# Kernel optimization log

Hardware: AMD Instinct MI355X
Metric: run time of the kernel (lower is better)

Reference implementation:

```python
import jax, jax.numpy as jnp
import numpy as np

GRID_H, GRID_W = 14, 14  # grid_size from init_kwargs (crop_height, crop_width)


def _bilinear_crop(feature_map, boxes, bbox_idx, crop_h, crop_w):
    """crop_and_resize-style ROIAlign.

    feature_map: [N, C, H, W] float
    boxes:       [M, 4] (x1, y1, x2, y2) in feature-map pixel coords
    bbox_idx:    [M] int32 batch index per box
    returns:     [M, C, crop_h, crop_w]
    """
    N, C, H, W = feature_map.shape
    x1, y1, x2, y2 = boxes[:, 0], boxes[:, 1], boxes[:, 2], boxes[:, 3]

    # Sample points evenly spaced INCLUDING the box corners (tf.crop_and_resize grid).
    ti = jnp.arange(crop_h, dtype=boxes.dtype) / (crop_h - 1)  # [gh]
    tj = jnp.arange(crop_w, dtype=boxes.dtype) / (crop_w - 1)  # [gw]
    ys = y1[:, None] + (y2 - y1)[:, None] * ti  # [M, gh]
    xs = x1[:, None] + (x2 - x1)[:, None] * tj  # [M, gw]

    # Out-of-range samples get extrapolation value 0.
    my = (ys >= 0) & (ys <= H - 1)  # [M, gh]
    mx = (xs >= 0) & (xs <= W - 1)  # [M, gw]

    y0f = jnp.floor(ys)
    x0f = jnp.floor(xs)
    ly = ys - y0f  # [M, gh] lerp weights
    lx = xs - x0f  # [M, gw]

    y0 = jnp.clip(y0f, 0, H - 1).astype(jnp.int32)
    y1i = jnp.clip(y0f + 1, 0, H - 1).astype(jnp.int32)
    x0 = jnp.clip(x0f, 0, W - 1).astype(jnp.int32)
    x1i = jnp.clip(x0f + 1, 0, W - 1).astype(jnp.int32)

    b = bbox_idx[:, None, None]            # [M,1,1]
    Y0, Y1 = y0[:, :, None], y1i[:, :, None]   # [M,gh,1]
    X0, X1 = x0[:, None, :], x1i[:, None, :]   # [M,1,gw]

    # Advanced indexing with the channel slice in the middle -> result [M,gh,gw,C]
    g00 = feature_map[b, :, Y0, X0]
    g01 = feature_map[b, :, Y0, X1]
    g10 = feature_map[b, :, Y1, X0]
    g11 = feature_map[b, :, Y1, X1]

    wy = ly[:, :, None, None]  # [M,gh,1,1]
    wx = lx[:, None, :, None]  # [M,1,gw,1]
    out = (g00 * (1 - wy) * (1 - wx) + g01 * (1 - wy) * wx
           + g10 * wy * (1 - wx) + g11 * wy * wx)  # [M,gh,gw,C]

    mask = (my[:, :, None] & mx[:, None, :])[..., None]  # [M,gh,gw,1]
    out = jnp.where(mask, out, jnp.zeros((), out.dtype))
    return jnp.transpose(out, (0, 3, 1, 2))  # [M,C,gh,gw]


def setup_inputs() -> dict:
    key = jax.random.key(0)
    k1, k2, k3, k4, k5, k6, k7 = jax.random.split(key, 7)
    N, C, H, W = 4, 256, 200, 200
    img = 800  # original image height/width; stride = img / H = 4
    M = 2048

    feature_map = jax.random.normal(k1, (N, C, H, W), dtype=jnp.float32)

    n = jax.random.randint(k2, (M,), 0, N).astype(jnp.float32)
    score = jax.random.uniform(k3, (M,), dtype=jnp.float32)
    x1 = jax.random.uniform(k4, (M,), dtype=jnp.float32, maxval=img * 0.6)
    y1 = jax.random.uniform(k5, (M,), dtype=jnp.float32, maxval=img * 0.6)
    bw = jax.random.uniform(k6, (M,), dtype=jnp.float32, minval=16.0, maxval=img * 0.4)
    bh = jax.random.uniform(k7, (M,), dtype=jnp.float32, minval=16.0, maxval=img * 0.4)
    x2 = jnp.minimum(x1 + bw, img - 1.0)
    y2 = jnp.minimum(y1 + bh, img - 1.0)

    rois = jnp.stack([n, score, x1, y1, x2, y2], axis=1)  # [M, 6]
    return {"feature_map": feature_map, "rois": rois, "img_height": img}


def reference(feature_map, rois, img_height):
    H = feature_map.shape[2]
    stride = img_height / H
    bbox_idx = rois[:, 0].astype(jnp.int32)
    boxes = rois[:, 2:] / stride  # image coords -> feature-map coords
    return _bilinear_crop(feature_map, boxes, bbox_idx, GRID_H, GRID_W)
```

## Files before the change

kernel.cpp:

```cpp
#include <hip/hip_runtime.h>

#define GH 14
#define GW 14

__global__ __launch_bounds__(256) void nchw_to_nhwc_kernel(
    const float* __restrict__ src, float* __restrict__ dst, int C, int HW)
{
    __shared__ float tile[32][33];
    const int b  = blockIdx.z;
    const int p0 = blockIdx.x * 32;
    const int c0 = blockIdx.y * 32;
    const int tx = threadIdx.x;
    const int ty = threadIdx.y;
    const float* s = src + (size_t)b * C * HW;
    float*       d = dst + (size_t)b * C * HW;
    #pragma unroll
    for (int k = 0; k < 4; ++k)
        tile[ty + k * 8][tx] = s[(size_t)(c0 + ty + k * 8) * HW + p0 + tx];
    __syncthreads();
    #pragma unroll
    for (int k = 0; k < 4; ++k)
        d[(size_t)(p0 + ty + k * 8) * C + c0 + tx] = tile[tx][ty + k * 8];
}

__global__ __launch_bounds__(256) void roi_gather_nhwc_kernel(
    const float* __restrict__ fmapT,
    const float* __restrict__ rois,
    const int*   __restrict__ imgh,
    float*       __restrict__ out,
    int C, int H, int W)
{
    __shared__ float lds[64 * 197];
    const int tid  = threadIdx.x;
    const int lane = tid & 63;
    const int wv   = tid >> 6;
    const int m    = blockIdx.y;
    const int c0   = blockIdx.x * 64;

    const float stride = (float)imgh[0] / (float)H;
    const float* r = rois + (size_t)m * 6;
    const int   b   = (int)r[0];
    const float rx1 = r[2] / stride;
    const float ry1 = r[3] / stride;
    const float rx2 = r[4] / stride;
    const float ry2 = r[5] / stride;

    const float* __restrict__ base = fmapT + (size_t)b * H * W * C + c0 + lane;

    const float fH = (float)(H - 1), fW = (float)(W - 1);

    #pragma unroll 2
    for (int k = 0; k < 49; ++k) {
        const int s = wv * 49 + k;
        const int i = s / GW;
        const int j = s - i * GW;

        const float ys = ry1 + (ry2 - ry1) * ((float)i / (float)(GH - 1));
        const float xs = rx1 + (rx2 - rx1) * ((float)j / (float)(GW - 1));

        const bool my = (ys >= 0.0f) && (ys <= fH);
        const bool mx = (xs >= 0.0f) && (xs <= fW);

        const float y0f = floorf(ys);
        const float x0f = floorf(xs);
        const float ly  = ys - y0f;
        const float lx  = xs - x0f;

        const int y0  = (int)fminf(fmaxf(y0f,        0.0f), fH);
        const int y1i = (int)fminf(fmaxf(y0f + 1.0f, 0.0f), fH);
        const int x0  = (int)fminf(fmaxf(x0f,        0.0f), fW);
        const int x1i = (int)fminf(fmaxf(x0f + 1.0f, 0.0f), fW);

        const float msk = (my && mx) ? 1.0f : 0.0f;
        const float w00 = msk * (1.0f - ly) * (1.0f - lx);
        const float w01 = msk * (1.0f - ly) * lx;
        const float w10 = msk * ly * (1.0f - lx);
        const float w11 = msk * ly * lx;

        const int o00 = (y0  * W + x0 ) * C;
        const int o01 = (y0  * W + x1i) * C;
        const int o10 = (y1i * W + x0 ) * C;
        const int o11 = (y1i * W + x1i) * C;
        const float g00 = base[o00];
        const float g01 = base[o01];
        const float g10 = base[o10];
        const float g11 = base[o11];

        lds[lane * 197 + s] = g00 * w00 + g01 * w01 + g10 * w10 + g11 * w11;
    }
    __syncthreads();

    for (int k = tid; k < 64 * GH * GW; k += 256) {
        const int ch = k / (GH * GW);
        const int s  = k - ch * (GH * GW);
        out[((size_t)m * C + c0 + ch) * (GH * GW) + s] = lds[ch * 197 + s];
    }
}

#define CCHUNK 64
__global__ __launch_bounds__(256) void roi_align_fallback(
    const float* __restrict__ fmap, const float* __restrict__ rois,
    const int* __restrict__ imgh, float* __restrict__ out, int C, int H, int W)
{
    const int t = threadIdx.x;
    if (t >= GH * GW) return;
    const int m = blockIdx.y;
    const int c0 = blockIdx.x * CCHUNK;
    const int j = t % GW;
    const int i = t / GW;
    const float stride = (float)imgh[0] / (float)H;
    const float* r = rois + (size_t)m * 6;
    const int b = (int)r[0];
    const float x1 = r[2] / stride, y1 = r[3] / stride;
    const float x2 = r[4] / stride, y2 = r[5] / stride;
    const float ys = y1 + (y2 - y1) * ((float)i / (float)(GH - 1));
    const float xs = x1 + (x2 - x1) * ((float)j / (float)(GW - 1));
    const bool my = (ys >= 0.0f) && (ys <= (float)(H - 1));
    const bool mx = (xs >= 0.0f) && (xs <= (float)(W - 1));
    const float y0f = floorf(ys), x0f = floorf(xs);
    const float ly = ys - y0f, lx = xs - x0f;
    const int y0  = (int)fminf(fmaxf(y0f,        0.0f), (float)(H - 1));
    const int y1i = (int)fminf(fmaxf(y0f + 1.0f, 0.0f), (float)(H - 1));
    const int x0  = (int)fminf(fmaxf(x0f,        0.0f), (float)(W - 1));
    const int x1i = (int)fminf(fmaxf(x0f + 1.0f, 0.0f), (float)(W - 1));
    const float msk = (my && mx) ? 1.0f : 0.0f;
    const float w00 = msk * (1.0f - ly) * (1.0f - lx);
    const float w01 = msk * (1.0f - ly) * lx;
    const float w10 = msk * ly * (1.0f - lx);
    const float w11 = msk * ly * lx;
    const int o00 = y0 * W + x0, o01 = y0 * W + x1i;
    const int o10 = y1i * W + x0, o11 = y1i * W + x1i;
    const int HW = H * W;
    const float* __restrict__ p = fmap + ((size_t)b * C + c0) * (size_t)HW;
    float* __restrict__ o = out + ((size_t)m * C + c0) * (size_t)(GH * GW) + t;
    #pragma unroll 4
    for (int c = 0; c < CCHUNK; ++c) {
        const float g00 = p[o00], g01 = p[o01], g10 = p[o10], g11 = p[o11];
        *o = g00 * w00 + g01 * w01 + g10 * w10 + g11 * w11;
        p += HW; o += GH * GW;
    }
}

extern "C" void kernel_launch(void* const* d_in, const int* in_sizes, int n_in,
                              void* d_out, int out_size, void* d_ws, size_t ws_size,
                              hipStream_t stream) {
    const float* fmap = (const float*)d_in[0];
    const float* rois = (const float*)d_in[1];
    const int*   imgh = (const int*)d_in[2];
    float* out = (float*)d_out;

    const int C = 256, H = 200, W = 200, N = 4;
    const int M  = in_sizes[1] / 6;
    const int HW = H * W;

    const size_t need = (size_t)N * C * HW * sizeof(float);
    if (ws_size >= need) {
        float* fmapT = (float*)d_ws;
        dim3 tgrid(HW / 32, C / 32, N);
        nchw_to_nhwc_kernel<<<tgrid, dim3(32, 8), 0, stream>>>(fmap, fmapT, C, HW);
        dim3 ggrid(C / 64, M);
        roi_gather_nhwc_kernel<<<ggrid, 256, 0, stream>>>(fmapT, rois, imgh, out, C, H, W);
    } else {
        dim3 grid(C / CCHUNK, M);
        roi_align_fallback<<<grid, 256, 0, stream>>>(fmap, rois, imgh, out, C, H, W);
    }
}
```

Before: 737.9 us.

## Gather all channels per ROI with float4 loads and precomputed sample tables

The gather kernel now runs one block per ROI covering all 256 channels. Sample offsets and bilinear weights are computed once into LDS tables, and each lane loads float4 vectors of four channels. Results are staged in LDS in passes of 28 samples, then transposed to write float4 rows of the NCHW output. This cuts redundant coordinate math and issues wider gather loads, at the cost of fewer, larger blocks and extra barriers per pass.

```diff
diff --git a/kernel.cpp b/kernel.cpp
--- a/kernel.cpp
+++ b/kernel.cpp
@@ -2,6 +2,9 @@
 
 #define GH 14
 #define GW 14
+#define GSAMP (GH * GW)
+#define PASS_S 28
+#define STG_STRIDE 260
 
 __global__ __launch_bounds__(256) void nchw_to_nhwc_kernel(
     const float* __restrict__ src, float* __restrict__ dst, int C, int HW)
@@ -23,19 +26,21 @@
         d[(size_t)(p0 + ty + k * 8) * C + c0 + tx] = tile[tx][ty + k * 8];
 }
 
-__global__ __launch_bounds__(256) void roi_gather_nhwc_kernel(
+__global__ __launch_bounds__(256, 4) void roi_gather_nhwc_kernel(
     const float* __restrict__ fmapT,
     const float* __restrict__ rois,
     const int*   __restrict__ imgh,
     float*       __restrict__ out,
     int C, int H, int W)
 {
-    __shared__ float lds[64 * 197];
+    __shared__ int4   s_oq[GSAMP];
+    __shared__ float4 s_w[GSAMP];
+    __shared__ float  stage[PASS_S * STG_STRIDE];
+
     const int tid  = threadIdx.x;
     const int lane = tid & 63;
     const int wv   = tid >> 6;
-    const int m    = blockIdx.y;
-    const int c0   = blockIdx.x * 64;
+    const int m    = blockIdx.x;
 
     const float stride = (float)imgh[0] / (float)H;
     const float* r = rois + (size_t)m * 6;
@@ -45,55 +50,72 @@
     const float rx2 = r[4] / stride;
     const float ry2 = r[5] / stride;
 
-    const float* __restrict__ base = fmapT + (size_t)b * H * W * C + c0 + lane;
-
+    const int C4 = C >> 2;
     const float fH = (float)(H - 1), fW = (float)(W - 1);
 
-    #pragma unroll 2
-    for (int k = 0; k < 49; ++k) {
-        const int s = wv * 49 + k;
-        const int i = s / GW;
-        const int j = s - i * GW;
-
+    if (tid < GSAMP) {
+        const int i = tid / GW;
+        const int j = tid - i * GW;
         const float ys = ry1 + (ry2 - ry1) * ((float)i / (float)(GH - 1));
         const float xs = rx1 + (rx2 - rx1) * ((float)j / (float)(GW - 1));
-
         const bool my = (ys >= 0.0f) && (ys <= fH);
         const bool mx = (xs >= 0.0f) && (xs <= fW);
-
         const float y0f = floorf(ys);
         const float x0f = floorf(xs);
         const float ly  = ys - y0f;
         const float lx  = xs - x0f;
-
         const int y0  = (int)fminf(fmaxf(y0f,        0.0f), fH);
         const int y1i = (int)fminf(fmaxf(y0f + 1.0f, 0.0f), fH);
         const int x0  = (int)fminf(fmaxf(x0f,        0.0f), fW);
         const int x1i = (int)fminf(fmaxf(x0f + 1.0f, 0.0f), fW);
-
         const float msk = (my && mx) ? 1.0f : 0.0f;
-        const float w00 = msk * (1.0f - ly) * (1.0f - lx);
-        const float w01 = msk * (1.0f - ly) * lx;
-        const float w10 = msk * ly * (1.0f - lx);
-        const float w11 = msk * ly * lx;
-
-        const int o00 = (y0  * W + x0 ) * C;
-        const int o01 = (y0  * W + x1i) * C;
-        const int o10 = (y1i * W + x0 ) * C;
-        const int o11 = (y1i * W + x1i) * C;
-        const float g00 = base[o00];
-        const float g01 = base[o01];
-        const float g10 = base[o10];
-        const float g11 = base[o11];
-
-        lds[lane * 197 + s] = g00 * w00 + g01 * w01 + g10 * w10 + g11 * w11;
+        s_w[tid]  = make_float4(msk * (1.0f - ly) * (1.0f - lx),
+                                msk * (1.0f - ly) * lx,
+                                msk * ly * (1.0f - lx),
+                                msk * ly * lx);
+        s_oq[tid] = make_int4((y0  * W + x0 ) * C4,
+                              (y0  * W + x1i) * C4,
+                              (y1i * W + x0 ) * C4,
+                              (y1i * W + x1i) * C4);
     }
     __syncthreads();
 
-    for (int k = tid; k < 64 * GH * GW; k += 256) {
-        const int ch = k / (GH * GW);
-        const int s  = k - ch * (GH * GW);
-        out[((size_t)m * C + c0 + ch) * (GH * GW) + s] = lds[ch * 197 + s];
+    const float4* __restrict__ bp =
+        (const float4*)fmapT + (size_t)b * (size_t)(H * W) * C4 + lane;
+
+    for (int pass = 0; pass < GSAMP / PASS_S; ++pass) {
+        #pragma unroll 2
+        for (int q = 0; q < PASS_S / 4; ++q) {
+            const int sl = wv * (PASS_S / 4) + q;
+            const int sg = pass * PASS_S + sl;
+            const int4   oq = s_oq[sg];
+            const float4 w  = s_w[sg];
+            const float4 g00 = bp[oq.x];
+            const float4 g01 = bp[oq.y];
+            const float4 g10 = bp[oq.z];
+            const float4 g11 = bp[oq.w];
+            float4 acc;
+            acc.x = g00.x * w.x + g01.x * w.y + g10.x * w.z + g11.x * w.w;
+            acc.y = g00.y * w.x + g01.y * w.y + g10.y * w.z + g11.y * w.w;
+            acc.z = g00.z * w.x + g01.z * w.y + g10.z * w.z + g11.z * w.w;
+            acc.w = g00.w * w.x + g01.w * w.y + g10.w * w.z + g11.w * w.w;
+            *(float4*)&stage[sl * STG_STRIDE + 4 * lane] = acc;
+        }
+        __syncthreads();
+
+        #pragma unroll
+        for (int it = 0; it < 7; ++it) {
+            const int e4 = tid + 256 * it;
+            const int ch = e4 / 7;
+            const int sq = e4 - 7 * ch;
+            float4 v;
+            v.x = stage[(4 * sq + 0) * STG_STRIDE + ch];
+            v.y = stage[(4 * sq + 1) * STG_STRIDE + ch];
+            v.z = stage[(4 * sq + 2) * STG_STRIDE + ch];
+            v.w = stage[(4 * sq + 3) * STG_STRIDE + ch];
+            *(float4*)(out + ((size_t)m * C + ch) * GSAMP + pass * PASS_S + 4 * sq) = v;
+        }
+        __syncthreads();
     }
 }
 
@@ -158,8 +180,7 @@
         float* fmapT = (float*)d_ws;
         dim3 tgrid(HW / 32, C / 32, N);
         nchw_to_nhwc_kernel<<<tgrid, dim3(32, 8), 0, stream>>>(fmap, fmapT, C, HW);
-        dim3 ggrid(C / 64, M);
-        roi_gather_nhwc_kernel<<<ggrid, 256, 0, stream>>>(fmapT, rois, imgh, out, C, H, W);
+        roi_gather_nhwc_kernel<<<dim3(M), 256, 0, stream>>>(fmapT, rois, imgh, out, C, H, W);
     } else {
         dim3 grid(C / CCHUNK, M);
         roi_align_fallback<<<grid, 256, 0, stream>>>(fmap, rois, imgh, out, C, H, W);
```

Measured after the change: 776.0 us. +5.2%, slower.
